# Kernel tuning notes

Measured on AMD Instinct MI355X. Metric: run time of the kernel, lower is better.

The kernel has to match this reference:

```python
import jax, jax.numpy as jnp
import numpy as np

B, L = 4096, 4096  # batch of spectra, spectrum length
MIN_W, MAX_W = 1024, 3072  # ragged overlap-window lengths


def setup_inputs() -> dict:
    key = jax.random.key(0)
    k1, k2, k3, k4, k5, k6 = jax.random.split(key, 6)
    fluctuate = jax.random.normal(k1, (B, 1, L), dtype=jnp.float32)
    ivar = jax.random.uniform(k2, (B, 1, L), dtype=jnp.float32)
    output = jax.random.normal(k3, (B, 1, L), dtype=jnp.float32)
    # per-sample window length and valid starts in both input and output
    lens = jax.random.randint(k4, (B,), MIN_W, MAX_W + 1)
    s_in = jax.random.randint(k5, (B,), 0, L - lens + 1)
    s_out = jax.random.randint(k6, (B,), 0, L - lens + 1)
    overlap_index = jnp.stack([s_in, s_in + lens, s_out, s_out + lens], axis=1).astype(jnp.int64)
    return {"fluctuate": fluctuate, "ivar": ivar, "output": output, "overlap_index": overlap_index}


def reference(fluctuate, ivar, output, overlap_index):
    # fluctuate/ivar: [B,1,L]; output: [B,1,Lo]; overlap_index: [B,4] = [s_in, e_in, s_out, e_out]
    Bn, _, Ln = fluctuate.shape
    Lo = output.shape[-1]
    s_in = overlap_index[:, 0]
    e_in = overlap_index[:, 1]
    s_out = overlap_index[:, 2]
    lens = e_in - s_in  # equal to e_out - s_out by construction

    j = jnp.arange(Ln)                           # [L] padded window positions
    mask = j[None, :] < lens[:, None]            # [B,L] valid positions
    idx_in = jnp.clip(s_in[:, None] + j[None, :], 0, Ln - 1)   # [B,L]
    idx_out = jnp.clip(s_out[:, None] + j[None, :], 0, Lo - 1)  # [B,L]

    x = jnp.take_along_axis(fluctuate[:, 0, :], idx_in, axis=1)
    w = jnp.take_along_axis(ivar[:, 0, :], idx_in, axis=1)
    y = jnp.take_along_axis(output[:, 0, :], idx_out, axis=1)

    sq = jnp.where(mask, (x - y) ** 2 * w, jnp.float32(0))
    per_sample = sq.sum(axis=1) / lens.astype(sq.dtype)  # mean over each ragged window
    return per_sample.mean()
```

## Files before the change

### kernel.cpp

```cpp
#include <hip/hip_runtime.h>

#define BLOCK 256

typedef float f4u __attribute__((ext_vector_type(4), aligned(4)));

__global__ __launch_bounds__(BLOCK, 8) void chi2_fused(
    const float* __restrict__ fluct,
    const float* __restrict__ ivar,
    const float* __restrict__ outp,
    const int*  __restrict__ ovl,
    float* __restrict__ out,
    int L, float inv_B)
{
    const int gwave = (blockIdx.x * BLOCK + threadIdx.x) >> 6;
    const int lane  = threadIdx.x & 63;
    const int b     = gwave >> 1;
    const int h     = gwave & 1;

    const int4 o   = reinterpret_cast<const int4*>(ovl)[b];
    const int s_in = o.x, e_in = o.y, s_out = o.z;
    const int len  = e_in - s_in;

    const float* __restrict__ xp = fluct + (size_t)b * L + s_in;
    const float* __restrict__ wp = ivar  + (size_t)b * L + s_in;
    const float* __restrict__ yp = outp  + (size_t)b * L + s_out;

    const int n4 = len >> 2;

    float a0 = 0.f, a1 = 0.f;
    int c = lane + (h << 6);
    for (; c + 128 < n4; c += 256) {
        const f4u xv0 = *reinterpret_cast<const f4u*>(xp + 4 * c);
        const f4u xv1 = *reinterpret_cast<const f4u*>(xp + 4 * (c + 128));
        const f4u yv0 = *reinterpret_cast<const f4u*>(yp + 4 * c);
        const f4u yv1 = *reinterpret_cast<const f4u*>(yp + 4 * (c + 128));
        const f4u wv0 = *reinterpret_cast<const f4u*>(wp + 4 * c);
        const f4u wv1 = *reinterpret_cast<const f4u*>(wp + 4 * (c + 128));
        #pragma unroll
        for (int e = 0; e < 4; ++e) {
            const float d0 = xv0[e] - yv0[e];
            const float d1 = xv1[e] - yv1[e];
            a0 = fmaf(d0 * d0, wv0[e], a0);
            a1 = fmaf(d1 * d1, wv1[e], a1);
        }
    }
    for (; c < n4; c += 128) {
        const f4u xv = *reinterpret_cast<const f4u*>(xp + 4 * c);
        const f4u yv = *reinterpret_cast<const f4u*>(yp + 4 * c);
        const f4u wv = *reinterpret_cast<const f4u*>(wp + 4 * c);
        #pragma unroll
        for (int e = 0; e < 4; ++e) {
            const float d = xv[e] - yv[e];
            a0 = fmaf(d * d, wv[e], a0);
        }
    }
    if (h) {
        const int done = n4 << 2;
        if (lane < (len & 3)) {
            const float d = xp[done + lane] - yp[done + lane];
            a0 = fmaf(d * d, wp[done + lane], a0);
        }
    }

    float acc = a0 + a1;

    #pragma unroll
    for (int off = 32; off > 0; off >>= 1)
        acc += __shfl_down(acc, off, 64);

    __shared__ float sacc[BLOCK / 64];
    if (lane == 0) sacc[threadIdx.x >> 6] = (acc / (float)len) * inv_B;
    __syncthreads();

    if (threadIdx.x == 0) {
        float s = 0.f;
        #pragma unroll
        for (int i = 0; i < BLOCK / 64; ++i) s += sacc[i];
        atomicAdd(out, s);
    }
}

extern "C" void kernel_launch(void* const* d_in, const int* in_sizes, int n_in,
                              void* d_out, int out_size, void* d_ws, size_t ws_size,
                              hipStream_t stream) {
    const float* fluct = (const float*)d_in[0];
    const float* ivar  = (const float*)d_in[1];
    const float* outp  = (const float*)d_in[2];
    const int*   ovl   = (const int*)d_in[3];

    const int B = in_sizes[3] / 4;
    const int L = in_sizes[0] / B;

    hipMemsetAsync(d_out, 0, sizeof(float) * out_size, stream);

    const int waves_per_block = BLOCK / 64;
    const int total_waves = B * 2;
    chi2_fused<<<total_waves / waves_per_block, BLOCK, 0, stream>>>(
        fluct, ivar, outp, ovl, (float*)d_out, L, 1.0f / (float)B);
}
```

Measured before the change: 186.3 us.

## Use one wave per sample with 4-way unrolled nontemporal loads

Each sample is now handled by a single wave instead of two half-waves, and the main loop is unrolled four ways with four independent accumulators. All streaming loads become nontemporal, and the launch bound's minimum-occupancy hint is dropped. The aim is more memory-level parallelism per wave and less cache pollution. The cost is half as many waves in flight, which may hurt latency hiding on a bandwidth-bound kernel.

```diff
diff --git a/kernel.cpp b/kernel.cpp
--- a/kernel.cpp
+++ b/kernel.cpp
@@ -4,7 +4,11 @@
 
 typedef float f4u __attribute__((ext_vector_type(4), aligned(4)));
 
-__global__ __launch_bounds__(BLOCK, 8) void chi2_fused(
+__device__ __forceinline__ f4u ntload(const float* p) {
+    return __builtin_nontemporal_load(reinterpret_cast<const f4u*>(p));
+}
+
+__global__ __launch_bounds__(BLOCK) void chi2_fused(
     const float* __restrict__ fluct,
     const float* __restrict__ ivar,
     const float* __restrict__ outp,
@@ -12,57 +16,63 @@
     float* __restrict__ out,
     int L, float inv_B)
 {
-    const int gwave = (blockIdx.x * BLOCK + threadIdx.x) >> 6;
-    const int lane  = threadIdx.x & 63;
-    const int b     = gwave >> 1;
-    const int h     = gwave & 1;
+    const int wave = (blockIdx.x * BLOCK + threadIdx.x) >> 6;
+    const int lane = threadIdx.x & 63;
 
-    const int4 o   = reinterpret_cast<const int4*>(ovl)[b];
+    const int4 o   = reinterpret_cast<const int4*>(ovl)[wave];
     const int s_in = o.x, e_in = o.y, s_out = o.z;
     const int len  = e_in - s_in;
 
-    const float* __restrict__ xp = fluct + (size_t)b * L + s_in;
-    const float* __restrict__ wp = ivar  + (size_t)b * L + s_in;
-    const float* __restrict__ yp = outp  + (size_t)b * L + s_out;
+    const float* __restrict__ xp = fluct + (size_t)wave * L + s_in;
+    const float* __restrict__ wp = ivar  + (size_t)wave * L + s_in;
+    const float* __restrict__ yp = outp  + (size_t)wave * L + s_out;
 
     const int n4 = len >> 2;
 
-    float a0 = 0.f, a1 = 0.f;
-    int c = lane + (h << 6);
-    for (; c + 128 < n4; c += 256) {
-        const f4u xv0 = *reinterpret_cast<const f4u*>(xp + 4 * c);
-        const f4u xv1 = *reinterpret_cast<const f4u*>(xp + 4 * (c + 128));
-        const f4u yv0 = *reinterpret_cast<const f4u*>(yp + 4 * c);
-        const f4u yv1 = *reinterpret_cast<const f4u*>(yp + 4 * (c + 128));
-        const f4u wv0 = *reinterpret_cast<const f4u*>(wp + 4 * c);
-        const f4u wv1 = *reinterpret_cast<const f4u*>(wp + 4 * (c + 128));
+    float a0 = 0.f, a1 = 0.f, a2 = 0.f, a3 = 0.f;
+    int c = lane;
+    for (; c + 192 < n4; c += 256) {
+        const f4u xv0 = ntload(xp + 4 * c);
+        const f4u xv1 = ntload(xp + 4 * (c +  64));
+        const f4u xv2 = ntload(xp + 4 * (c + 128));
+        const f4u xv3 = ntload(xp + 4 * (c + 192));
+        const f4u yv0 = ntload(yp + 4 * c);
+        const f4u yv1 = ntload(yp + 4 * (c +  64));
+        const f4u yv2 = ntload(yp + 4 * (c + 128));
+        const f4u yv3 = ntload(yp + 4 * (c + 192));
+        const f4u wv0 = ntload(wp + 4 * c);
+        const f4u wv1 = ntload(wp + 4 * (c +  64));
+        const f4u wv2 = ntload(wp + 4 * (c + 128));
+        const f4u wv3 = ntload(wp + 4 * (c + 192));
         #pragma unroll
         for (int e = 0; e < 4; ++e) {
             const float d0 = xv0[e] - yv0[e];
             const float d1 = xv1[e] - yv1[e];
+            const float d2 = xv2[e] - yv2[e];
+            const float d3 = xv3[e] - yv3[e];
             a0 = fmaf(d0 * d0, wv0[e], a0);
             a1 = fmaf(d1 * d1, wv1[e], a1);
+            a2 = fmaf(d2 * d2, wv2[e], a2);
+            a3 = fmaf(d3 * d3, wv3[e], a3);
         }
     }
-    for (; c < n4; c += 128) {
-        const f4u xv = *reinterpret_cast<const f4u*>(xp + 4 * c);
-        const f4u yv = *reinterpret_cast<const f4u*>(yp + 4 * c);
-        const f4u wv = *reinterpret_cast<const f4u*>(wp + 4 * c);
+    for (; c < n4; c += 64) {
+        const f4u xv = ntload(xp + 4 * c);
+        const f4u yv = ntload(yp + 4 * c);
+        const f4u wv = ntload(wp + 4 * c);
         #pragma unroll
         for (int e = 0; e < 4; ++e) {
             const float d = xv[e] - yv[e];
             a0 = fmaf(d * d, wv[e], a0);
         }
     }
-    if (h) {
-        const int done = n4 << 2;
-        if (lane < (len & 3)) {
-            const float d = xp[done + lane] - yp[done + lane];
-            a0 = fmaf(d * d, wp[done + lane], a0);
-        }
+    const int done = n4 << 2;
+    if (lane < (len & 3)) {
+        const float d = xp[done + lane] - yp[done + lane];
+        a0 = fmaf(d * d, wp[done + lane], a0);
     }
 
-    float acc = a0 + a1;
+    float acc = (a0 + a1) + (a2 + a3);
 
     #pragma unroll
     for (int off = 32; off > 0; off >>= 1)
@@ -94,7 +104,6 @@
     hipMemsetAsync(d_out, 0, sizeof(float) * out_size, stream);
 
     const int waves_per_block = BLOCK / 64;
-    const int total_waves = B * 2;
-    chi2_fused<<<total_waves / waves_per_block, BLOCK, 0, stream>>>(
+    chi2_fused<<<B / waves_per_block, BLOCK, 0, stream>>>(
         fluct, ivar, outp, ovl, (float*)d_out, L, 1.0f / (float)B);
 }
```

Result: faster. 172.5 us (-7.4%).
